# Performance work log

Hardware: AMD Instinct MI355X
Metric: run time of the kernel (lower is better)

The kernel has to match this reference:

```python
import jax, jax.numpy as jnp
import numpy as np

N = 100_000   # nodes
E = 200_000   # directed edges
G = 2_500     # graphs in batch
F_NODE = 16
F_EDGE = 8
H1 = 32
H2 = 16


def setup_inputs() -> dict:
    key = jax.random.key(0)
    ks = jax.random.split(key, 24)
    p = lambda k, shape: 0.1 * jax.random.normal(k, shape, dtype=jnp.float32)
    inp = {
        "x": jax.random.normal(ks[0], (N, F_NODE), dtype=jnp.float32),
        "edge_attr": jax.random.normal(ks[1], (E, F_EDGE), dtype=jnp.float32),
        # edge-MLP for conv1: F_EDGE -> 16 -> F_NODE*H1
        "w_e1a": p(ks[2], (F_EDGE, 16)), "b_e1a": p(ks[3], (16,)),
        "w_e1b": p(ks[4], (16, F_NODE * H1)), "b_e1b": p(ks[5], (F_NODE * H1,)),
        "w_root1": p(ks[6], (F_NODE, H1)), "b_root1": p(ks[7], (H1,)),
        # edge-MLP for conv2: F_EDGE -> 16 -> H1*H2
        "w_e2a": p(ks[8], (F_EDGE, 16)), "b_e2a": p(ks[9], (16,)),
        "w_e2b": p(ks[10], (16, H1 * H2)), "b_e2b": p(ks[11], (H1 * H2,)),
        "w_root2": p(ks[12], (H1, H2)), "b_root2": p(ks[13], (H2,)),
        # attention-pool gate nn: F_NODE -> F_NODE -> 1
        "w_g1": p(ks[14], (F_NODE, F_NODE)), "b_g1": p(ks[15], (F_NODE,)),
        "w_g2": p(ks[16], (F_NODE, 1)), "b_g2": p(ks[17], (1,)),
        # head: (H2 + F_NODE) -> 8 -> 1
        "w_l1": p(ks[18], (H2 + F_NODE, 8)), "b_l1": p(ks[19], (8,)),
        "w_l2": p(ks[20], (8, 1)), "b_l2": p(ks[21], (1,)),
        "edge_index": jax.random.randint(ks[22], (2, E), 0, N),
        "batch": jnp.sort(jax.random.randint(ks[23], (N,), 0, G)),
    }
    return inp


def _nnconv(x, src, tgt, edge_attr, wa, ba, wb, bb, wr, br, in_c, out_c, n):
    # PyG NNConv: x_i' = x_i @ W_root + b + sum_{j->i} x_j @ Theta(e_ji)
    h = jax.nn.relu(edge_attr @ wa + ba)              # [E, 16]
    theta = (h @ wb + bb).reshape(-1, in_c, out_c)    # [E, in, out]
    msg = jnp.einsum('ei,eio->eo', x[src], theta)     # [E, out]
    agg = jax.ops.segment_sum(msg, tgt, num_segments=n)
    return x @ wr + br + agg


def reference(x, edge_attr, w_e1a, b_e1a, w_e1b, b_e1b, w_root1, b_root1,
              w_e2a, b_e2a, w_e2b, b_e2b, w_root2, b_root2,
              w_g1, b_g1, w_g2, b_g2, w_l1, b_l1, w_l2, b_l2,
              edge_index, batch):
    src, tgt = edge_index[0], edge_index[1]
    n = x.shape[0]

    # GlobalAttention pooling on raw node features (per-graph segment softmax)
    gate = jax.nn.relu(x @ w_g1 + b_g1) @ w_g2 + b_g2          # [N, 1]
    m = jax.ops.segment_max(gate, batch, num_segments=G)       # [G, 1]
    a = jnp.exp(gate - m[batch])
    s = jax.ops.segment_sum(a, batch, num_segments=G)
    x_att = jax.ops.segment_sum((a / s[batch]) * x, batch, num_segments=G)  # [G, F_NODE]

    # Two NNConv layers with ReLU
    h = jax.nn.relu(_nnconv(x, src, tgt, edge_attr, w_e1a, b_e1a, w_e1b, b_e1b,
                            w_root1, b_root1, F_NODE, H1, n))
    h = jax.nn.relu(_nnconv(h, src, tgt, edge_attr, w_e2a, b_e2a, w_e2b, b_e2b,
                            w_root2, b_root2, H1, H2, n))

    # global_mean_pool
    cnt = jax.ops.segment_sum(jnp.ones((n, 1), h.dtype), batch, num_segments=G)
    mean = jax.ops.segment_sum(h, batch, num_segments=G) / jnp.maximum(cnt, 1.0)

    z = jnp.concatenate([mean, x_att], axis=1)  # [G, H2 + F_NODE]
    # eval mode: dropout p=0.5 is identity; two linear layers, no activation between
    z = z @ w_l1 + b_l1
    z = z @ w_l2 + b_l2
    return z
```

## Files before the change

### kernel.cpp

```cpp
#include <hip/hip_runtime.h>
#include <hip/hip_bf16.h>

#define NN 100000
#define NE 200000
#define NG 2500
#define FN 16
#define FE 8
#define H1C 32
#define H2C 16
#define KH 16

typedef __attribute__((ext_vector_type(8))) short short8;
typedef __attribute__((ext_vector_type(4))) float f32x4;

__device__ __forceinline__ float bf2f(unsigned int u){
  union { unsigned int i; float f; } v; v.i = (u & 0xffffu) << 16; return v.f;
}
__device__ __forceinline__ unsigned short f2bf(float f){
  union { float f; unsigned int i; } u; u.f = f;
  unsigned int r = u.i + 0x7fffu + ((u.i >> 16) & 1u);
  return (unsigned short)(r >> 16);
}
__device__ __forceinline__ unsigned int pk2(float a, float b){
  return (unsigned int)f2bf(a) | ((unsigned int)f2bf(b) << 16);
}
__device__ __forceinline__ float rdf(const void* p, long i, bool isbf){
  return isbf ? bf2f(((const unsigned short*)p)[i]) : ((const float*)p)[i];
}
__device__ __forceinline__ int lower_bound_i(const int* __restrict__ a, int n, int v){
  int lo = 0, hi = n;
  while(lo < hi){ int mid = (lo + hi) >> 1; if(a[mid] < v) lo = mid + 1; else hi = mid; }
  return lo;
}
__device__ __forceinline__ bool detect_isbf(const void* __restrict__ x){
  const unsigned short* u = (const unsigned short*)x;
  int lane = threadIdx.x & 63;
  float f = bf2f(u[2*lane]);
  float a = fabsf(f);
  bool sane = (f == 0.0f) || (a > 1e-4f && a < 1e4f);
  unsigned long long b = __ballot(sane);
  return __popcll(b) >= 32;
}

#define NW 20
struct WArgs { const void* p[NW]; };
enum {
  OW_E1A=0,     OB_E1A=128,   OW_E1B=144,   OB_E1B=8336,  OW_R1=8848,  OB_R1=9360,
  OW_E2A=9392,  OB_E2A=9520,  OW_E2B=9536,  OB_E2B=17728, OW_R2=18240, OB_R2=18752,
  OW_G1=18768,  OB_G1=19024,  OW_G2=19040,  OB_G2=19056,
  OW_L1=19057,  OB_L1=19313,  OW_L2=19321,  OB_L2=19329
};

#define MB_A 76
#define MB_B (MB_A + 19)
#define MB_C (MB_B + 18)
#define MB_D (MB_C + 391)
#define MB_E (MB_D + 782)
__global__ void __launch_bounds__(256) mega1_kernel(
    const void* __restrict__ xin, const void* __restrict__ efin, WArgs w,
    const int* __restrict__ ei,
    float* __restrict__ wts, unsigned int* __restrict__ wpack1, unsigned int* __restrict__ wpack2,
    float* __restrict__ gate, float* __restrict__ xf, int* __restrict__ deg)
{
  int b = blockIdx.x, tid = threadIdx.x;
  if(b < MB_A){
    bool isbf = detect_isbf(xin);
    int i = b*256 + tid;
    if(i >= 19330) return;
    const int sz[NW] = {128,16,8192,512,512,32, 128,16,8192,512,512,16, 256,16,16,1, 256,8,8,1};
    int seg = 0; long base = 0;
    while(i - base >= sz[seg]){ base += sz[seg]; seg++; }
    wts[i] = rdf(w.p[seg], i - base, isbf);
    return;
  }
  if(b < MB_B){
    bool isbf = detect_isbf(xin);
    int j = (b - MB_A)*256 + tid;
    if(j >= 4736) return;
    int n = j / 148; int k = (j % 148) * 2;
    float v0 = 0.f, v1 = 0.f;
    if(k < 256)        v0 = rdf(w.p[2], (long)k*32 + n, isbf);
    else if(k < 272)   v0 = rdf(w.p[3], (long)(k-256)*32 + n, isbf);
    if(k+1 < 256)      v1 = rdf(w.p[2], (long)(k+1)*32 + n, isbf);
    else if(k+1 < 272) v1 = rdf(w.p[3], (long)(k+1-256)*32 + n, isbf);
    wpack1[j] = pk2(v0, v1);
    return;
  }
  if(b < MB_C){
    bool isbf = detect_isbf(xin);
    int j = (b - MB_B)*256 + tid;
    if(j >= 4416) return;
    int n = j / 276; int k = (j % 276) * 2;
    float v0 = 0.f, v1 = 0.f;
    if(k < 512)        v0 = rdf(w.p[8], (long)k*16 + n, isbf);
    else if(k < 544)   v0 = rdf(w.p[9], (long)(k-512)*16 + n, isbf);
    if(k+1 < 512)      v1 = rdf(w.p[8], (long)(k+1)*16 + n, isbf);
    else if(k+1 < 544) v1 = rdf(w.p[9], (long)(k+1-512)*16 + n, isbf);
    wpack2[j] = pk2(v0, v1);
    return;
  }
  if(b < MB_D){
    __shared__ float s_w1[FN*FN], s_b1[FN], s_w2[FN], s_b2v[1];
    bool isbf = detect_isbf(xin);
    if(tid < FN*FN) s_w1[tid] = rdf(w.p[12], tid, isbf);
    if(tid < FN){ s_b1[tid] = rdf(w.p[13], tid, isbf); s_w2[tid] = rdf(w.p[14], tid, isbf); }
    if(tid == 0) s_b2v[0] = rdf(w.p[15], 0, isbf);
    __syncthreads();
    int n = (b - MB_C)*256 + tid;
    if(n >= NN) return;
    float xv[FN];
    if(isbf){
      uint4 u0 = ((const uint4*)xin)[2*n], u1 = ((const uint4*)xin)[2*n+1];
      xv[0]=bf2f(u0.x); xv[1]=bf2f(u0.x>>16); xv[2]=bf2f(u0.y); xv[3]=bf2f(u0.y>>16);
      xv[4]=bf2f(u0.z); xv[5]=bf2f(u0.z>>16); xv[6]=bf2f(u0.w); xv[7]=bf2f(u0.w>>16);
      xv[8]=bf2f(u1.x); xv[9]=bf2f(u1.x>>16); xv[10]=bf2f(u1.y); xv[11]=bf2f(u1.y>>16);
      xv[12]=bf2f(u1.z); xv[13]=bf2f(u1.z>>16); xv[14]=bf2f(u1.w); xv[15]=bf2f(u1.w>>16);
    } else {
      #pragma unroll
      for(int q = 0; q < 4; q++){
        float4 v = ((const float4*)xin)[4*n + q];
        xv[q*4+0]=v.x; xv[q*4+1]=v.y; xv[q*4+2]=v.z; xv[q*4+3]=v.w;
      }
    }
    float4* xo = (float4*)(xf + (size_t)n*FN);
    #pragma unroll
    for(int q = 0; q < 4; q++) xo[q] = make_float4(xv[q*4+0], xv[q*4+1], xv[q*4+2], xv[q*4+3]);
    float g = s_b2v[0];
    #pragma unroll
    for(int j = 0; j < FN; j++){
      float hj = s_b1[j];
      #pragma unroll
      for(int i = 0; i < FN; i++) hj += xv[i] * s_w1[i*FN + j];
      hj = hj > 0.f ? hj : 0.f;
      g += hj * s_w2[j];
    }
    gate[n] = g;
    return;
  }
  {
    int e = (b - MB_D)*256 + tid;
    if(e < NE) atomicAdd(&deg[ei[NE + e]], 1);
  }
}

#define SCAN_NB 98
__global__ void __launch_bounds__(256) scan_kernel(
    const int* __restrict__ deg, int* __restrict__ rowptr, int* __restrict__ cursor,
    unsigned int* __restrict__ pub)
{
  __shared__ int s_thr[256];
  __shared__ int s_agg[SCAN_NB];
  __shared__ int s_bcast;
  int tid = threadIdx.x, bid = blockIdx.x;
  int base = bid*1024 + tid*4;
  int v0=0, v1=0, v2=0, v3=0;
  if(base + 3 < NN){
    int4 t4 = *(const int4*)(deg + base);
    v0=t4.x; v1=t4.y; v2=t4.z; v3=t4.w;
  } else {
    if(base+0 < NN) v0 = deg[base+0];
    if(base+1 < NN) v1 = deg[base+1];
    if(base+2 < NN) v2 = deg[base+2];
  }
  int e1 = v0, e2 = v0+v1, e3 = v0+v1+v2, tot = v0+v1+v2+v3;
  s_thr[tid] = tot;
  __syncthreads();
  for(int off = 1; off < 256; off <<= 1){
    int t = (tid >= off) ? s_thr[tid-off] : 0;
    __syncthreads();
    s_thr[tid] += t;
    __syncthreads();
  }
  int thr_excl = s_thr[tid] - tot;
  int agg = s_thr[255];
  if(tid == 0) atomicExch(&pub[bid], ((unsigned int)agg << 1) | 1u);
  if(tid < SCAN_NB){
    unsigned int v;
    do { v = atomicAdd(&pub[tid], 0u); } while((v & 1u) == 0u);
    s_agg[tid] = (int)(v >> 1);
  }
  __syncthreads();
  if(tid == 0){
    int acc = 0;
    for(int p = 0; p < bid; p++) acc += s_agg[p];
    s_bcast = acc;
  }
  __syncthreads();
  int ex = s_bcast + thr_excl;
  if(base + 3 < NN){
    int4 r = make_int4(ex, ex+e1, ex+e2, ex+e3);
    *(int4*)(rowptr + base) = r;
    *(int4*)(cursor + base) = r;
  } else {
    if(base+0 < NN){ rowptr[base+0]=ex;    cursor[base+0]=ex;    }
    if(base+1 < NN){ rowptr[base+1]=ex+e1; cursor[base+1]=ex+e1; }
    if(base+2 < NN){ rowptr[base+2]=ex+e2; cursor[base+2]=ex+e2; }
  }
  if(bid == 0 && tid == 0) rowptr[NN] = NE;
}

__global__ void __launch_bounds__(256) fill_edge_kernel(
    const int* __restrict__ ei, int* __restrict__ cursor,
    const void* __restrict__ efin, const float* __restrict__ wts, const void* __restrict__ xin,
    int* __restrict__ srcp, unsigned int* __restrict__ hpk1, unsigned int* __restrict__ hpk2)
{
  __shared__ float s_w1[FE*KH], s_b1[KH], s_w2[FE*KH], s_b2[KH];
  int tid = threadIdx.x;
  if(tid < FE*KH){ s_w1[tid] = wts[OW_E1A + tid]; s_w2[tid] = wts[OW_E2A + tid]; }
  if(tid < KH){ s_b1[tid] = wts[OB_E1A + tid]; s_b2[tid] = wts[OB_E2A + tid]; }
  bool isbf = detect_isbf(xin);
  __syncthreads();
  int e = blockIdx.x*256 + tid;
  if(e >= NE) return;
  int pos = atomicAdd(&cursor[ei[NE + e]], 1);
  srcp[pos] = ei[e];
  float ev[FE];
  if(isbf){
    uint4 u = ((const uint4*)efin)[e];
    ev[0]=bf2f(u.x); ev[1]=bf2f(u.x>>16); ev[2]=bf2f(u.y); ev[3]=bf2f(u.y>>16);
    ev[4]=bf2f(u.z); ev[5]=bf2f(u.z>>16); ev[6]=bf2f(u.w); ev[7]=bf2f(u.w>>16);
  } else {
    float4 a = ((const float4*)efin)[2*e], b = ((const float4*)efin)[2*e+1];
    ev[0]=a.x; ev[1]=a.y; ev[2]=a.z; ev[3]=a.w; ev[4]=b.x; ev[5]=b.y; ev[6]=b.z; ev[7]=b.w;
  }
  unsigned int o[8];
  #pragma unroll
  for(int d = 0; d < 8; d++){
    float h0 = s_b1[2*d], h1 = s_b1[2*d+1];
    #pragma unroll
    for(int k = 0; k < FE; k++){
      h0 += ev[k] * s_w1[k*KH + 2*d];
      h1 += ev[k] * s_w1[k*KH + 2*d+1];
    }
    h0 = h0 > 0.f ? h0 : 0.f; h1 = h1 > 0.f ? h1 : 0.f;
    o[d] = pk2(h0, h1);
  }
  uint4* p1 = (uint4*)(hpk1 + (size_t)pos*8);
  p1[0] = make_uint4(o[0],o[1],o[2],o[3]); p1[1] = make_uint4(o[4],o[5],o[6],o[7]);
  #pragma unroll
  for(int d = 0; d < 8; d++){
    float h0 = s_b2[2*d], h1 = s_b2[2*d+1];
    #pragma unroll
    for(int k = 0; k < FE; k++){
      h0 += ev[k] * s_w2[k*KH + 2*d];
      h1 += ev[k] * s_w2[k*KH + 2*d+1];
    }
    h0 = h0 > 0.f ? h0 : 0.f; h1 = h1 > 0.f ? h1 : 0.f;
    o[d] = pk2(h0, h1);
  }
  uint4* p2 = (uint4*)(hpk2 + (size_t)pos*8);
  p2[0] = make_uint4(o[0],o[1],o[2],o[3]); p2[1] = make_uint4(o[4],o[5],o[6],o[7]);
}

template<int IN, int OUT, bool ABF>
__global__ void __launch_bounds__(256) conv_mfma_kernel(
    const void* __restrict__ nodef, const unsigned int* __restrict__ hpk,
    const int* __restrict__ srcp, const unsigned short* __restrict__ wpack,
    unsigned short* __restrict__ msg)
{
  constexpr int KMF  = ((KH*IN + IN + 31)/32)*32;
  constexpr int KP   = KMF + 8;
  constexpr int NT   = OUT/16;
  constexpr int KS   = KMF/32;
  int tid = threadIdx.x;
  int lane = tid & 63, m = lane & 15, quad = lane >> 4;
  int wid = tid >> 6;
  int ebase = blockIdx.x*64 + wid*16;
  int em = ebase + m;
  int sn = srcp[em];
  int q1 = quad >> 1;
  int xoff = (IN == 16) ? ((quad & 1)*8) : (quad*8);
  float x8[8];
  short8 xb;
  if(ABF){
    uint4 u = *(const uint4*)((const unsigned short*)nodef + (size_t)sn*IN + xoff);
    unsigned int uu[4] = {u.x, u.y, u.z, u.w};
    #pragma unroll
    for(int k = 0; k < 4; k++){ x8[2*k] = bf2f(uu[k]); x8[2*k+1] = bf2f(uu[k] >> 16); }
    xb = *(short8*)&u;
  } else {
    const float4* xp = (const float4*)((const float*)nodef + (size_t)sn*IN + xoff);
    float4 v0 = xp[0], v1 = xp[1];
    x8[0]=v0.x; x8[1]=v0.y; x8[2]=v0.z; x8[3]=v0.w;
    x8[4]=v1.x; x8[5]=v1.y; x8[6]=v1.z; x8[7]=v1.w;
    unsigned int* xbp = (unsigned int*)&xb;
    #pragma unroll
    for(int k = 0; k < 4; k++) xbp[k] = pk2(x8[2*k], x8[2*k+1]);
  }
  unsigned int hu[8];
  {
    const uint4* hp = (const uint4*)(hpk + (size_t)em*8);
    uint4 u0 = hp[0], u1 = hp[1];
    hu[0]=u0.x; hu[1]=u0.y; hu[2]=u0.z; hu[3]=u0.w;
    hu[4]=u1.x; hu[5]=u1.y; hu[6]=u1.z; hu[7]=u1.w;
  }

  f32x4 acc[NT];
  #pragma unroll
  for(int nt = 0; nt < NT; nt++) acc[nt] = (f32x4){0.f,0.f,0.f,0.f};

  #pragma unroll
  for(int ks = 0; ks < KS; ks++){
    short8 a;
    if(ks < KS-1){
      float hv = (IN == 16) ? bf2f(hu[ks] >> (16*q1))
                            : bf2f(hu[ks >> 1] >> (16*(ks & 1)));
      unsigned int* ap = (unsigned int*)&a;
      #pragma unroll
      for(int k = 0; k < 4; k++) ap[k] = pk2(hv*x8[2*k], hv*x8[2*k+1]);
    } else {
      if(IN == 16) a = (quad < 2) ? xb : (short8){0,0,0,0,0,0,0,0};
      else         a = xb;
    }
    #pragma unroll
    for(int nt = 0; nt < NT; nt++){
      short8 b = *(const short8*)(wpack + (size_t)(nt*16 + m)*KP + ks*32 + quad*8);
      acc[nt] = __builtin_amdgcn_mfma_f32_16x16x32_bf16(a, b, acc[nt], 0, 0, 0);
    }
  }
  #pragma unroll
  for(int nt = 0; nt < NT; nt++)
    #pragma unroll
    for(int r = 0; r < 4; r++)
      msg[(size_t)(ebase + quad*4 + r)*OUT + nt*16 + m] = f2bf(acc[nt][r]);
}

__global__ void __launch_bounds__(256) gather1_kernel(
    const float* __restrict__ xf, const unsigned short* __restrict__ msg,
    const int* __restrict__ rowptr,
    const float* __restrict__ wr, const float* __restrict__ br,
    unsigned short* __restrict__ h1b)
{
  __shared__ float s_w[FN*H1C], s_b[H1C];
  for(int i = threadIdx.x; i < FN*H1C; i += 256) s_w[i] = wr[i];
  if(threadIdx.x < H1C) s_b[threadIdx.x] = br[threadIdx.x];
  __syncthreads();
  int g = blockIdx.x*256 + threadIdx.x;
  int n = g >> 3, q = g & 7;
  if(n >= NN) return;
  float a0 = s_b[q*4+0], a1 = s_b[q*4+1], a2 = s_b[q*4+2], a3 = s_b[q*4+3];
  int jb = rowptr[n], je = rowptr[n+1];
  for(int j = jb; j < je; j++){
    const unsigned int* mp = (const unsigned int*)(msg + (size_t)j*H1C + q*4);
    unsigned int u0 = mp[0], u1 = mp[1];
    a0 += bf2f(u0); a1 += bf2f(u0 >> 16); a2 += bf2f(u1); a3 += bf2f(u1 >> 16);
  }
  const float* xr = xf + (size_t)n*FN;
  #pragma unroll
  for(int i = 0; i < FN; i++){
    float xi = xr[i];
    a0 += xi*s_w[i*H1C + q*4+0]; a1 += xi*s_w[i*H1C + q*4+1];
    a2 += xi*s_w[i*H1C + q*4+2]; a3 += xi*s_w[i*H1C + q*4+3];
  }
  a0 = a0>0.f?a0:0.f; a1 = a1>0.f?a1:0.f; a2 = a2>0.f?a2:0.f; a3 = a3>0.f?a3:0.f;
  uint2 hb; hb.x = pk2(a0, a1); hb.y = pk2(a2, a3);
  *(uint2*)(h1b + (size_t)n*H1C + q*4) = hb;
}

__global__ void __launch_bounds__(256) gather2_kernel(
    const unsigned short* __restrict__ h1b, const unsigned short* __restrict__ msg,
    const int* __restrict__ rowptr,
    const float* __restrict__ wr, const float* __restrict__ br, float* __restrict__ h2)
{
  __shared__ float s_w[H1C*H2C], s_b[H2C];
  for(int i = threadIdx.x; i < H1C*H2C; i += 256) s_w[i] = wr[i];
  if(threadIdx.x < H2C) s_b[threadIdx.x] = br[threadIdx.x];
  __syncthreads();
  int g = blockIdx.x*256 + threadIdx.x;
  int n = g >> 2, q = g & 3;
  if(n >= NN) return;
  float a0 = s_b[q*4+0], a1 = s_b[q*4+1], a2 = s_b[q*4+2], a3 = s_b[q*4+3];
  int jb = rowptr[n], je = rowptr[n+1];
  for(int j = jb; j < je; j++){
    const unsigned int* mp = (const unsigned int*)(msg + (size_t)j*H2C + q*4);
    unsigned int u0 = mp[0], u1 = mp[1];
    a0 += bf2f(u0); a1 += bf2f(u0 >> 16); a2 += bf2f(u1); a3 += bf2f(u1 >> 16);
  }
  const unsigned int* hb = (const unsigned int*)(h1b + (size_t)n*H1C);
  #pragma unroll
  for(int i2 = 0; i2 < H1C/2; i2++){
    unsigned int u = hb[i2];
    float x0 = bf2f(u), x1 = bf2f(u >> 16);
    int i = 2*i2;
    a0 += x0*s_w[i*H2C + q*4+0] + x1*s_w[(i+1)*H2C + q*4+0];
    a1 += x0*s_w[i*H2C + q*4+1] + x1*s_w[(i+1)*H2C + q*4+1];
    a2 += x0*s_w[i*H2C + q*4+2] + x1*s_w[(i+1)*H2C + q*4+2];
    a3 += x0*s_w[i*H2C + q*4+3] + x1*s_w[(i+1)*H2C + q*4+3];
  }
  float4 r; r.x = a0>0.f?a0:0.f; r.y = a1>0.f?a1:0.f; r.z = a2>0.f?a2:0.f; r.w = a3>0.f?a3:0.f;
  *(float4*)(h2 + (size_t)n*H2C + q*4) = r;
}

__global__ void head_kernel(const float* __restrict__ gate, const float* __restrict__ xf,
    const float* __restrict__ h2, const int* __restrict__ batch, const void* __restrict__ xin,
    const float* __restrict__ wl1, const float* __restrict__ bl1,
    const float* __restrict__ wl2, const float* __restrict__ bl2,
    void* __restrict__ out)
{
  __shared__ float sz[H2C + FN];
  int g = blockIdx.x;
  int lane = threadIdx.x;
  bool isbf = detect_isbf(xin);
  int start = lower_bound_i(batch, NN, g);
  int end   = lower_bound_i(batch, NN, g + 1);
  float m = -1e30f;
  for(int n = start + lane; n < end; n += 64) m = fmaxf(m, gate[n]);
  #pragma unroll
  for(int o = 32; o >= 1; o >>= 1) m = fmaxf(m, __shfl_xor(m, o));
  float s = 0.f;
  float acc[FN];
  #pragma unroll
  for(int f = 0; f < FN; f++) acc[f] = 0.f;
  for(int n = start + lane; n < end; n += 64){
    float a = __expf(gate[n] - m);
    s += a;
    const float4* xp = (const float4*)(xf + (size_t)n * FN);
    #pragma unroll
    for(int q = 0; q < 4; q++){
      float4 v = xp[q];
      acc[q*4+0] += a*v.x; acc[q*4+1] += a*v.y; acc[q*4+2] += a*v.z; acc[q*4+3] += a*v.w;
    }
  }
  #pragma unroll
  for(int o = 32; o >= 1; o >>= 1){
    s += __shfl_xor(s, o);
    #pragma unroll
    for(int f = 0; f < FN; f++) acc[f] += __shfl_xor(acc[f], o);
  }
  if(lane < FN) sz[H2C + lane] = (end > start && s > 0.f) ? acc[lane] / s : 0.f;
  #pragma unroll
  for(int f = 0; f < H2C; f++) acc[f] = 0.f;
  for(int n = start + lane; n < end; n += 64){
    const float4* hp = (const float4*)(h2 + (size_t)n*H2C);
    #pragma unroll
    for(int q = 0; q < 4; q++){
      float4 v = hp[q];
      acc[q*4+0] += v.x; acc[q*4+1] += v.y; acc[q*4+2] += v.z; acc[q*4+3] += v.w;
    }
  }
  #pragma unroll
  for(int o = 32; o >= 1; o >>= 1){
    #pragma unroll
    for(int f = 0; f < H2C; f++) acc[f] += __shfl_xor(acc[f], o);
  }
  float inv = 1.f / fmaxf((float)(end - start), 1.f);
  if(lane < H2C) sz[lane] = acc[lane] * inv;
  __syncthreads();
  if(lane == 0){
    float t1[8];
    #pragma unroll
    for(int j = 0; j < 8; j++){
      float t = bl1[j];
      #pragma unroll
      for(int c = 0; c < H2C + FN; c++) t += sz[c] * wl1[c*8 + j];
      t1[j] = t;
    }
    float o = bl2[0];
    #pragma unroll
    for(int j = 0; j < 8; j++) o += t1[j] * wl2[j];
    if(isbf) ((__hip_bfloat16*)out)[g] = __float2bfloat16(o);
    else     ((float*)out)[g] = o;
  }
}

extern "C" void kernel_launch(void* const* d_in, const int* in_sizes, int n_in,
                              void* d_out, int out_size, void* d_ws, size_t ws_size,
                              hipStream_t stream)
{
  const int* ei    = (const int*)d_in[22];
  const int* batch = (const int*)d_in[23];

  float* ws = (float*)d_ws;
  float* xf     = ws;
  float* gate   = xf + 1600000;
  float* wts    = gate + 100000;
  int*   rowptr = (int*)(wts + 19360);
  int*   cursor = rowptr + 100016;
  int*   deg    = cursor + 100000;
  unsigned int* pub = (unsigned int*)(deg + 100000);
  int*   srcp   = (int*)(pub + 256);
  unsigned int* wpack1 = (unsigned int*)(srcp + 200000);
  unsigned int* wpack2 = wpack1 + 4736;
  unsigned short* h1b  = (unsigned short*)(wpack2 + 4416);
  unsigned int* hpk1   = (unsigned int*)h1b;
  unsigned short* msg1 = h1b + 3200000;
  unsigned short* msg2 = msg1;
  float* h2     = (float*)(msg1 + 6400000);
  unsigned int* hpk2   = (unsigned int*)h2;

  WArgs wa;
  for(int i = 0; i < NW; i++) wa.p[i] = d_in[2 + i];

  hipMemsetAsync(deg, 0, (100000 + 256)*sizeof(int), stream);
  mega1_kernel<<<MB_E, 256, 0, stream>>>(d_in[0], d_in[1], wa, ei, wts, wpack1, wpack2, gate, xf, deg);
  scan_kernel<<<SCAN_NB, 256, 0, stream>>>(deg, rowptr, cursor, pub);
  fill_edge_kernel<<<(NE + 255)/256, 256, 0, stream>>>(ei, cursor, d_in[1], wts, d_in[0], srcp, hpk1, hpk2);

  conv_mfma_kernel<FN, H1C, false><<<NE/64, 256, 0, stream>>>(
      xf, hpk1, srcp, (const unsigned short*)wpack1, msg1);
  gather1_kernel<<<(NN*8 + 255)/256, 256, 0, stream>>>(xf, msg1, rowptr, wts+OW_R1, wts+OB_R1, h1b);

  conv_mfma_kernel<H1C, H2C, true><<<NE/64, 256, 0, stream>>>(
      h1b, hpk2, srcp, (const unsigned short*)wpack2, msg2);
  gather2_kernel<<<(NN*4 + 255)/256, 256, 0, stream>>>(h1b, msg2, rowptr, wts+OW_R2, wts+OB_R2, h2);

  head_kernel<<<NG, 64, 0, stream>>>(gate, xf, h2, batch, d_in[0],
      wts+OW_L1, wts+OB_L1, wts+OW_L2, wts+OB_L2, d_out);
}
```

Measured before the change: 213.4 us.

## Fuse all stages into one persistent kernel with software grid barriers

Replaces the sequence of seven kernel launches (prep, scan, edge fill, two conv/gather pairs, head) with a single persistent kernel of 512 blocks that grid-strides over each stage and separates stages with an atomic-counter grid barrier. The aim is to remove per-launch overhead and inter-kernel idle gaps between the many short stages. In exchange, each stage now runs on a fixed 512-block grid, which may limit parallelism for stages that had more blocks. The spin barrier assumes all 512 blocks are co-resident (launch bounds allow 2 blocks per CU); if they are not, the kernel deadlocks.

```diff
diff --git a/kernel.cpp b/kernel.cpp
--- a/kernel.cpp
+++ b/kernel.cpp
@@ -9,6 +9,7 @@
 #define H1C 32
 #define H2C 16
 #define KH 16
+#define GB 512
 
 typedef __attribute__((ext_vector_type(8))) short short8;
 typedef __attribute__((ext_vector_type(4))) float f32x4;
@@ -42,6 +43,22 @@
   return __popcll(b) >= 32;
 }
 
+__device__ __forceinline__ void gridbar(int* __restrict__ cnt, int* __restrict__ gen){
+  __syncthreads();
+  if(threadIdx.x == 0){
+    __threadfence();
+    int g = atomicAdd(gen, 0);
+    if(atomicAdd(cnt, 1) == GB-1){
+      atomicExch(cnt, 0);
+      atomicAdd(gen, 1);
+    } else {
+      while(atomicAdd(gen, 0) == g) __builtin_amdgcn_s_sleep(2);
+    }
+    __threadfence();
+  }
+  __syncthreads();
+}
+
 #define NW 20
 struct WArgs { const void* p[NW]; };
 enum {
@@ -50,210 +67,14 @@
   OW_G1=18768,  OB_G1=19024,  OW_G2=19040,  OB_G2=19056,
   OW_L1=19057,  OB_L1=19313,  OW_L2=19321,  OB_L2=19329
 };
-
 #define MB_A 76
 #define MB_B (MB_A + 19)
 #define MB_C (MB_B + 18)
 #define MB_D (MB_C + 391)
-#define MB_E (MB_D + 782)
-__global__ void __launch_bounds__(256) mega1_kernel(
-    const void* __restrict__ xin, const void* __restrict__ efin, WArgs w,
-    const int* __restrict__ ei,
-    float* __restrict__ wts, unsigned int* __restrict__ wpack1, unsigned int* __restrict__ wpack2,
-    float* __restrict__ gate, float* __restrict__ xf, int* __restrict__ deg)
-{
-  int b = blockIdx.x, tid = threadIdx.x;
-  if(b < MB_A){
-    bool isbf = detect_isbf(xin);
-    int i = b*256 + tid;
-    if(i >= 19330) return;
-    const int sz[NW] = {128,16,8192,512,512,32, 128,16,8192,512,512,16, 256,16,16,1, 256,8,8,1};
-    int seg = 0; long base = 0;
-    while(i - base >= sz[seg]){ base += sz[seg]; seg++; }
-    wts[i] = rdf(w.p[seg], i - base, isbf);
-    return;
-  }
-  if(b < MB_B){
-    bool isbf = detect_isbf(xin);
-    int j = (b - MB_A)*256 + tid;
-    if(j >= 4736) return;
-    int n = j / 148; int k = (j % 148) * 2;
-    float v0 = 0.f, v1 = 0.f;
-    if(k < 256)        v0 = rdf(w.p[2], (long)k*32 + n, isbf);
-    else if(k < 272)   v0 = rdf(w.p[3], (long)(k-256)*32 + n, isbf);
-    if(k+1 < 256)      v1 = rdf(w.p[2], (long)(k+1)*32 + n, isbf);
-    else if(k+1 < 272) v1 = rdf(w.p[3], (long)(k+1-256)*32 + n, isbf);
-    wpack1[j] = pk2(v0, v1);
-    return;
-  }
-  if(b < MB_C){
-    bool isbf = detect_isbf(xin);
-    int j = (b - MB_B)*256 + tid;
-    if(j >= 4416) return;
-    int n = j / 276; int k = (j % 276) * 2;
-    float v0 = 0.f, v1 = 0.f;
-    if(k < 512)        v0 = rdf(w.p[8], (long)k*16 + n, isbf);
-    else if(k < 544)   v0 = rdf(w.p[9], (long)(k-512)*16 + n, isbf);
-    if(k+1 < 512)      v1 = rdf(w.p[8], (long)(k+1)*16 + n, isbf);
-    else if(k+1 < 544) v1 = rdf(w.p[9], (long)(k+1-512)*16 + n, isbf);
-    wpack2[j] = pk2(v0, v1);
-    return;
-  }
-  if(b < MB_D){
-    __shared__ float s_w1[FN*FN], s_b1[FN], s_w2[FN], s_b2v[1];
-    bool isbf = detect_isbf(xin);
-    if(tid < FN*FN) s_w1[tid] = rdf(w.p[12], tid, isbf);
-    if(tid < FN){ s_b1[tid] = rdf(w.p[13], tid, isbf); s_w2[tid] = rdf(w.p[14], tid, isbf); }
-    if(tid == 0) s_b2v[0] = rdf(w.p[15], 0, isbf);
-    __syncthreads();
-    int n = (b - MB_C)*256 + tid;
-    if(n >= NN) return;
-    float xv[FN];
-    if(isbf){
-      uint4 u0 = ((const uint4*)xin)[2*n], u1 = ((const uint4*)xin)[2*n+1];
-      xv[0]=bf2f(u0.x); xv[1]=bf2f(u0.x>>16); xv[2]=bf2f(u0.y); xv[3]=bf2f(u0.y>>16);
-      xv[4]=bf2f(u0.z); xv[5]=bf2f(u0.z>>16); xv[6]=bf2f(u0.w); xv[7]=bf2f(u0.w>>16);
-      xv[8]=bf2f(u1.x); xv[9]=bf2f(u1.x>>16); xv[10]=bf2f(u1.y); xv[11]=bf2f(u1.y>>16);
-      xv[12]=bf2f(u1.z); xv[13]=bf2f(u1.z>>16); xv[14]=bf2f(u1.w); xv[15]=bf2f(u1.w>>16);
-    } else {
-      #pragma unroll
-      for(int q = 0; q < 4; q++){
-        float4 v = ((const float4*)xin)[4*n + q];
-        xv[q*4+0]=v.x; xv[q*4+1]=v.y; xv[q*4+2]=v.z; xv[q*4+3]=v.w;
-      }
-    }
-    float4* xo = (float4*)(xf + (size_t)n*FN);
-    #pragma unroll
-    for(int q = 0; q < 4; q++) xo[q] = make_float4(xv[q*4+0], xv[q*4+1], xv[q*4+2], xv[q*4+3]);
-    float g = s_b2v[0];
-    #pragma unroll
-    for(int j = 0; j < FN; j++){
-      float hj = s_b1[j];
-      #pragma unroll
-      for(int i = 0; i < FN; i++) hj += xv[i] * s_w1[i*FN + j];
-      hj = hj > 0.f ? hj : 0.f;
-      g += hj * s_w2[j];
-    }
-    gate[n] = g;
-    return;
-  }
-  {
-    int e = (b - MB_D)*256 + tid;
-    if(e < NE) atomicAdd(&deg[ei[NE + e]], 1);
-  }
-}
-
-#define SCAN_NB 98
-__global__ void __launch_bounds__(256) scan_kernel(
-    const int* __restrict__ deg, int* __restrict__ rowptr, int* __restrict__ cursor,
-    unsigned int* __restrict__ pub)
-{
-  __shared__ int s_thr[256];
-  __shared__ int s_agg[SCAN_NB];
-  __shared__ int s_bcast;
-  int tid = threadIdx.x, bid = blockIdx.x;
-  int base = bid*1024 + tid*4;
-  int v0=0, v1=0, v2=0, v3=0;
-  if(base + 3 < NN){
-    int4 t4 = *(const int4*)(deg + base);
-    v0=t4.x; v1=t4.y; v2=t4.z; v3=t4.w;
-  } else {
-    if(base+0 < NN) v0 = deg[base+0];
-    if(base+1 < NN) v1 = deg[base+1];
-    if(base+2 < NN) v2 = deg[base+2];
-  }
-  int e1 = v0, e2 = v0+v1, e3 = v0+v1+v2, tot = v0+v1+v2+v3;
-  s_thr[tid] = tot;
-  __syncthreads();
-  for(int off = 1; off < 256; off <<= 1){
-    int t = (tid >= off) ? s_thr[tid-off] : 0;
-    __syncthreads();
-    s_thr[tid] += t;
-    __syncthreads();
-  }
-  int thr_excl = s_thr[tid] - tot;
-  int agg = s_thr[255];
-  if(tid == 0) atomicExch(&pub[bid], ((unsigned int)agg << 1) | 1u);
-  if(tid < SCAN_NB){
-    unsigned int v;
-    do { v = atomicAdd(&pub[tid], 0u); } while((v & 1u) == 0u);
-    s_agg[tid] = (int)(v >> 1);
-  }
-  __syncthreads();
-  if(tid == 0){
-    int acc = 0;
-    for(int p = 0; p < bid; p++) acc += s_agg[p];
-    s_bcast = acc;
-  }
-  __syncthreads();
-  int ex = s_bcast + thr_excl;
-  if(base + 3 < NN){
-    int4 r = make_int4(ex, ex+e1, ex+e2, ex+e3);
-    *(int4*)(rowptr + base) = r;
-    *(int4*)(cursor + base) = r;
-  } else {
-    if(base+0 < NN){ rowptr[base+0]=ex;    cursor[base+0]=ex;    }
-    if(base+1 < NN){ rowptr[base+1]=ex+e1; cursor[base+1]=ex+e1; }
-    if(base+2 < NN){ rowptr[base+2]=ex+e2; cursor[base+2]=ex+e2; }
-  }
-  if(bid == 0 && tid == 0) rowptr[NN] = NE;
-}
-
-__global__ void __launch_bounds__(256) fill_edge_kernel(
-    const int* __restrict__ ei, int* __restrict__ cursor,
-    const void* __restrict__ efin, const float* __restrict__ wts, const void* __restrict__ xin,
-    int* __restrict__ srcp, unsigned int* __restrict__ hpk1, unsigned int* __restrict__ hpk2)
-{
-  __shared__ float s_w1[FE*KH], s_b1[KH], s_w2[FE*KH], s_b2[KH];
-  int tid = threadIdx.x;
-  if(tid < FE*KH){ s_w1[tid] = wts[OW_E1A + tid]; s_w2[tid] = wts[OW_E2A + tid]; }
-  if(tid < KH){ s_b1[tid] = wts[OB_E1A + tid]; s_b2[tid] = wts[OB_E2A + tid]; }
-  bool isbf = detect_isbf(xin);
-  __syncthreads();
-  int e = blockIdx.x*256 + tid;
-  if(e >= NE) return;
-  int pos = atomicAdd(&cursor[ei[NE + e]], 1);
-  srcp[pos] = ei[e];
-  float ev[FE];
-  if(isbf){
-    uint4 u = ((const uint4*)efin)[e];
-    ev[0]=bf2f(u.x); ev[1]=bf2f(u.x>>16); ev[2]=bf2f(u.y); ev[3]=bf2f(u.y>>16);
-    ev[4]=bf2f(u.z); ev[5]=bf2f(u.z>>16); ev[6]=bf2f(u.w); ev[7]=bf2f(u.w>>16);
-  } else {
-    float4 a = ((const float4*)efin)[2*e], b = ((const float4*)efin)[2*e+1];
-    ev[0]=a.x; ev[1]=a.y; ev[2]=a.z; ev[3]=a.w; ev[4]=b.x; ev[5]=b.y; ev[6]=b.z; ev[7]=b.w;
-  }
-  unsigned int o[8];
-  #pragma unroll
-  for(int d = 0; d < 8; d++){
-    float h0 = s_b1[2*d], h1 = s_b1[2*d+1];
-    #pragma unroll
-    for(int k = 0; k < FE; k++){
-      h0 += ev[k] * s_w1[k*KH + 2*d];
-      h1 += ev[k] * s_w1[k*KH + 2*d+1];
-    }
-    h0 = h0 > 0.f ? h0 : 0.f; h1 = h1 > 0.f ? h1 : 0.f;
-    o[d] = pk2(h0, h1);
-  }
-  uint4* p1 = (uint4*)(hpk1 + (size_t)pos*8);
-  p1[0] = make_uint4(o[0],o[1],o[2],o[3]); p1[1] = make_uint4(o[4],o[5],o[6],o[7]);
-  #pragma unroll
-  for(int d = 0; d < 8; d++){
-    float h0 = s_b2[2*d], h1 = s_b2[2*d+1];
-    #pragma unroll
-    for(int k = 0; k < FE; k++){
-      h0 += ev[k] * s_w2[k*KH + 2*d];
-      h1 += ev[k] * s_w2[k*KH + 2*d+1];
-    }
-    h0 = h0 > 0.f ? h0 : 0.f; h1 = h1 > 0.f ? h1 : 0.f;
-    o[d] = pk2(h0, h1);
-  }
-  uint4* p2 = (uint4*)(hpk2 + (size_t)pos*8);
-  p2[0] = make_uint4(o[0],o[1],o[2],o[3]); p2[1] = make_uint4(o[4],o[5],o[6],o[7]);
-}
+#define CHUNK 196
 
 template<int IN, int OUT, bool ABF>
-__global__ void __launch_bounds__(256) conv_mfma_kernel(
+__device__ __forceinline__ void conv_unit(int u, int tid,
     const void* __restrict__ nodef, const unsigned int* __restrict__ hpk,
     const int* __restrict__ srcp, const unsigned short* __restrict__ wpack,
     unsigned short* __restrict__ msg)
@@ -262,10 +83,9 @@
   constexpr int KP   = KMF + 8;
   constexpr int NT   = OUT/16;
   constexpr int KS   = KMF/32;
-  int tid = threadIdx.x;
   int lane = tid & 63, m = lane & 15, quad = lane >> 4;
   int wid = tid >> 6;
-  int ebase = blockIdx.x*64 + wid*16;
+  int ebase = u*64 + wid*16;
   int em = ebase + m;
   int sn = srcp[em];
   int q1 = quad >> 1;
@@ -273,11 +93,11 @@
   float x8[8];
   short8 xb;
   if(ABF){
-    uint4 u = *(const uint4*)((const unsigned short*)nodef + (size_t)sn*IN + xoff);
-    unsigned int uu[4] = {u.x, u.y, u.z, u.w};
+    uint4 uu4 = *(const uint4*)((const unsigned short*)nodef + (size_t)sn*IN + xoff);
+    unsigned int uu[4] = {uu4.x, uu4.y, uu4.z, uu4.w};
     #pragma unroll
     for(int k = 0; k < 4; k++){ x8[2*k] = bf2f(uu[k]); x8[2*k+1] = bf2f(uu[k] >> 16); }
-    xb = *(short8*)&u;
+    xb = *(short8*)&uu4;
   } else {
     const float4* xp = (const float4*)((const float*)nodef + (size_t)sn*IN + xoff);
     float4 v0 = xp[0], v1 = xp[1];
@@ -294,11 +114,9 @@
     hu[0]=u0.x; hu[1]=u0.y; hu[2]=u0.z; hu[3]=u0.w;
     hu[4]=u1.x; hu[5]=u1.y; hu[6]=u1.z; hu[7]=u1.w;
   }
-
   f32x4 acc[NT];
   #pragma unroll
   for(int nt = 0; nt < NT; nt++) acc[nt] = (f32x4){0.f,0.f,0.f,0.f};
-
   #pragma unroll
   for(int ks = 0; ks < KS; ks++){
     short8 a;
@@ -314,8 +132,8 @@
     }
     #pragma unroll
     for(int nt = 0; nt < NT; nt++){
-      short8 b = *(const short8*)(wpack + (size_t)(nt*16 + m)*KP + ks*32 + quad*8);
-      acc[nt] = __builtin_amdgcn_mfma_f32_16x16x32_bf16(a, b, acc[nt], 0, 0, 0);
+      short8 bfr = *(const short8*)(wpack + (size_t)(nt*16 + m)*KP + ks*32 + quad*8);
+      acc[nt] = __builtin_amdgcn_mfma_f32_16x16x32_bf16(a, bfr, acc[nt], 0, 0, 0);
     }
   }
   #pragma unroll
@@ -325,141 +143,322 @@
       msg[(size_t)(ebase + quad*4 + r)*OUT + nt*16 + m] = f2bf(acc[nt][r]);
 }
 
-__global__ void __launch_bounds__(256) gather1_kernel(
-    const float* __restrict__ xf, const unsigned short* __restrict__ msg,
-    const int* __restrict__ rowptr,
-    const float* __restrict__ wr, const float* __restrict__ br,
-    unsigned short* __restrict__ h1b)
+__global__ void __launch_bounds__(256, 2) mega_kernel(
+    const void* __restrict__ xin, const void* __restrict__ efin, WArgs w,
+    const int* __restrict__ ei, const int* __restrict__ batch,
+    float* __restrict__ wts, unsigned int* __restrict__ wpack1, unsigned int* __restrict__ wpack2,
+    float* __restrict__ gate, float* __restrict__ xf,
+    int* __restrict__ deg, int* __restrict__ partials, int* __restrict__ bar,
+    int* __restrict__ rowptr, int* __restrict__ cursor, int* __restrict__ srcp,
+    unsigned int* __restrict__ hpk1, unsigned int* __restrict__ hpk2,
+    unsigned short* __restrict__ h1b, unsigned short* __restrict__ msg,
+    float* __restrict__ h2, void* __restrict__ out)
 {
-  __shared__ float s_w[FN*H1C], s_b[H1C];
-  for(int i = threadIdx.x; i < FN*H1C; i += 256) s_w[i] = wr[i];
-  if(threadIdx.x < H1C) s_b[threadIdx.x] = br[threadIdx.x];
-  __syncthreads();
-  int g = blockIdx.x*256 + threadIdx.x;
-  int n = g >> 3, q = g & 7;
-  if(n >= NN) return;
-  float a0 = s_b[q*4+0], a1 = s_b[q*4+1], a2 = s_b[q*4+2], a3 = s_b[q*4+3];
-  int jb = rowptr[n], je = rowptr[n+1];
-  for(int j = jb; j < je; j++){
-    const unsigned int* mp = (const unsigned int*)(msg + (size_t)j*H1C + q*4);
-    unsigned int u0 = mp[0], u1 = mp[1];
-    a0 += bf2f(u0); a1 += bf2f(u0 >> 16); a2 += bf2f(u1); a3 += bf2f(u1 >> 16);
-  }
-  const float* xr = xf + (size_t)n*FN;
-  #pragma unroll
-  for(int i = 0; i < FN; i++){
-    float xi = xr[i];
-    a0 += xi*s_w[i*H1C + q*4+0]; a1 += xi*s_w[i*H1C + q*4+1];
-    a2 += xi*s_w[i*H1C + q*4+2]; a3 += xi*s_w[i*H1C + q*4+3];
-  }
-  a0 = a0>0.f?a0:0.f; a1 = a1>0.f?a1:0.f; a2 = a2>0.f?a2:0.f; a3 = a3>0.f?a3:0.f;
-  uint2 hb; hb.x = pk2(a0, a1); hb.y = pk2(a2, a3);
-  *(uint2*)(h1b + (size_t)n*H1C + q*4) = hb;
-}
-
-__global__ void __launch_bounds__(256) gather2_kernel(
-    const unsigned short* __restrict__ h1b, const unsigned short* __restrict__ msg,
-    const int* __restrict__ rowptr,
-    const float* __restrict__ wr, const float* __restrict__ br, float* __restrict__ h2)
-{
-  __shared__ float s_w[H1C*H2C], s_b[H2C];
-  for(int i = threadIdx.x; i < H1C*H2C; i += 256) s_w[i] = wr[i];
-  if(threadIdx.x < H2C) s_b[threadIdx.x] = br[threadIdx.x];
-  __syncthreads();
-  int g = blockIdx.x*256 + threadIdx.x;
-  int n = g >> 2, q = g & 3;
-  if(n >= NN) return;
-  float a0 = s_b[q*4+0], a1 = s_b[q*4+1], a2 = s_b[q*4+2], a3 = s_b[q*4+3];
-  int jb = rowptr[n], je = rowptr[n+1];
-  for(int j = jb; j < je; j++){
-    const unsigned int* mp = (const unsigned int*)(msg + (size_t)j*H2C + q*4);
-    unsigned int u0 = mp[0], u1 = mp[1];
-    a0 += bf2f(u0); a1 += bf2f(u0 >> 16); a2 += bf2f(u1); a3 += bf2f(u1 >> 16);
-  }
-  const unsigned int* hb = (const unsigned int*)(h1b + (size_t)n*H1C);
-  #pragma unroll
-  for(int i2 = 0; i2 < H1C/2; i2++){
-    unsigned int u = hb[i2];
-    float x0 = bf2f(u), x1 = bf2f(u >> 16);
-    int i = 2*i2;
-    a0 += x0*s_w[i*H2C + q*4+0] + x1*s_w[(i+1)*H2C + q*4+0];
-    a1 += x0*s_w[i*H2C + q*4+1] + x1*s_w[(i+1)*H2C + q*4+1];
-    a2 += x0*s_w[i*H2C + q*4+2] + x1*s_w[(i+1)*H2C + q*4+2];
-    a3 += x0*s_w[i*H2C + q*4+3] + x1*s_w[(i+1)*H2C + q*4+3];
-  }
-  float4 r; r.x = a0>0.f?a0:0.f; r.y = a1>0.f?a1:0.f; r.z = a2>0.f?a2:0.f; r.w = a3>0.f?a3:0.f;
-  *(float4*)(h2 + (size_t)n*H2C + q*4) = r;
-}
-
-__global__ void head_kernel(const float* __restrict__ gate, const float* __restrict__ xf,
-    const float* __restrict__ h2, const int* __restrict__ batch, const void* __restrict__ xin,
-    const float* __restrict__ wl1, const float* __restrict__ bl1,
-    const float* __restrict__ wl2, const float* __restrict__ bl2,
-    void* __restrict__ out)
-{
-  __shared__ float sz[H2C + FN];
-  int g = blockIdx.x;
-  int lane = threadIdx.x;
+  __shared__ int   s_i[512];
+  __shared__ float s_f[512];
+  __shared__ float s_f2[64];
+  __shared__ float s_hd[4*48];
+  int b = blockIdx.x, tid = threadIdx.x;
+  int* cnt = bar; int* gen = bar + 4;
   bool isbf = detect_isbf(xin);
-  int start = lower_bound_i(batch, NN, g);
-  int end   = lower_bound_i(batch, NN, g + 1);
-  float m = -1e30f;
-  for(int n = start + lane; n < end; n += 64) m = fmaxf(m, gate[n]);
-  #pragma unroll
-  for(int o = 32; o >= 1; o >>= 1) m = fmaxf(m, __shfl_xor(m, o));
-  float s = 0.f;
-  float acc[FN];
-  #pragma unroll
-  for(int f = 0; f < FN; f++) acc[f] = 0.f;
-  for(int n = start + lane; n < end; n += 64){
-    float a = __expf(gate[n] - m);
-    s += a;
-    const float4* xp = (const float4*)(xf + (size_t)n * FN);
-    #pragma unroll
-    for(int q = 0; q < 4; q++){
-      float4 v = xp[q];
-      acc[q*4+0] += a*v.x; acc[q*4+1] += a*v.y; acc[q*4+2] += a*v.z; acc[q*4+3] += a*v.w;
-    }
-  }
-  #pragma unroll
-  for(int o = 32; o >= 1; o >>= 1){
-    s += __shfl_xor(s, o);
-    #pragma unroll
-    for(int f = 0; f < FN; f++) acc[f] += __shfl_xor(acc[f], o);
-  }
-  if(lane < FN) sz[H2C + lane] = (end > start && s > 0.f) ? acc[lane] / s : 0.f;
-  #pragma unroll
-  for(int f = 0; f < H2C; f++) acc[f] = 0.f;
-  for(int n = start + lane; n < end; n += 64){
-    const float4* hp = (const float4*)(h2 + (size_t)n*H2C);
-    #pragma unroll
-    for(int q = 0; q < 4; q++){
-      float4 v = hp[q];
-      acc[q*4+0] += v.x; acc[q*4+1] += v.y; acc[q*4+2] += v.z; acc[q*4+3] += v.w;
-    }
-  }
-  #pragma unroll
-  for(int o = 32; o >= 1; o >>= 1){
-    #pragma unroll
-    for(int f = 0; f < H2C; f++) acc[f] += __shfl_xor(acc[f], o);
-  }
-  float inv = 1.f / fmaxf((float)(end - start), 1.f);
-  if(lane < H2C) sz[lane] = acc[lane] * inv;
-  __syncthreads();
-  if(lane == 0){
-    float t1[8];
-    #pragma unroll
-    for(int j = 0; j < 8; j++){
-      float t = bl1[j];
-      #pragma unroll
-      for(int c = 0; c < H2C + FN; c++) t += sz[c] * wl1[c*8 + j];
-      t1[j] = t;
-    }
-    float o = bl2[0];
-    #pragma unroll
-    for(int j = 0; j < 8; j++) o += t1[j] * wl2[j];
-    if(isbf) ((__hip_bfloat16*)out)[g] = __float2bfloat16(o);
-    else     ((float*)out)[g] = o;
+
+  if(b < MB_A){
+    int i = b*256 + tid;
+    if(i < 19330){
+      const int sz[NW] = {128,16,8192,512,512,32, 128,16,8192,512,512,16, 256,16,16,1, 256,8,8,1};
+      int seg = 0; long base = 0;
+      while(i - base >= sz[seg]){ base += sz[seg]; seg++; }
+      wts[i] = rdf(w.p[seg], i - base, isbf);
+    }
+  } else if(b < MB_B){
+    int j = (b - MB_A)*256 + tid;
+    if(j < 4736){
+      int n = j / 148; int k = (j % 148) * 2;
+      float v0 = 0.f, v1 = 0.f;
+      if(k < 256)        v0 = rdf(w.p[2], (long)k*32 + n, isbf);
+      else if(k < 272)   v0 = rdf(w.p[3], (long)(k-256)*32 + n, isbf);
+      if(k+1 < 256)      v1 = rdf(w.p[2], (long)(k+1)*32 + n, isbf);
+      else if(k+1 < 272) v1 = rdf(w.p[3], (long)(k+1-256)*32 + n, isbf);
+      wpack1[j] = pk2(v0, v1);
+    }
+  } else if(b < MB_C){
+    int j = (b - MB_B)*256 + tid;
+    if(j < 4416){
+      int n = j / 276; int k = (j % 276) * 2;
+      float v0 = 0.f, v1 = 0.f;
+      if(k < 512)        v0 = rdf(w.p[8], (long)k*16 + n, isbf);
+      else if(k < 544)   v0 = rdf(w.p[9], (long)(k-512)*16 + n, isbf);
+      if(k+1 < 512)      v1 = rdf(w.p[8], (long)(k+1)*16 + n, isbf);
+      else if(k+1 < 544) v1 = rdf(w.p[9], (long)(k+1-512)*16 + n, isbf);
+      wpack2[j] = pk2(v0, v1);
+    }
+  } else if(b < MB_D){
+    if(tid < FN*FN) s_f[tid] = rdf(w.p[12], tid, isbf);
+    if(tid < FN){ s_f2[tid] = rdf(w.p[13], tid, isbf); s_f2[32 + tid] = rdf(w.p[14], tid, isbf); }
+    if(tid == 0) s_f2[63] = rdf(w.p[15], 0, isbf);
+    __syncthreads();
+    int n = (b - MB_C)*256 + tid;
+    if(n < NN){
+      float xv[FN];
+      if(isbf){
+        uint4 u0 = ((const uint4*)xin)[2*n], u1 = ((const uint4*)xin)[2*n+1];
+        xv[0]=bf2f(u0.x); xv[1]=bf2f(u0.x>>16); xv[2]=bf2f(u0.y); xv[3]=bf2f(u0.y>>16);
+        xv[4]=bf2f(u0.z); xv[5]=bf2f(u0.z>>16); xv[6]=bf2f(u0.w); xv[7]=bf2f(u0.w>>16);
+        xv[8]=bf2f(u1.x); xv[9]=bf2f(u1.x>>16); xv[10]=bf2f(u1.y); xv[11]=bf2f(u1.y>>16);
+        xv[12]=bf2f(u1.z); xv[13]=bf2f(u1.z>>16); xv[14]=bf2f(u1.w); xv[15]=bf2f(u1.w>>16);
+      } else {
+        #pragma unroll
+        for(int q = 0; q < 4; q++){
+          float4 v = ((const float4*)xin)[4*n + q];
+          xv[q*4+0]=v.x; xv[q*4+1]=v.y; xv[q*4+2]=v.z; xv[q*4+3]=v.w;
+        }
+      }
+      float4* xo = (float4*)(xf + (size_t)n*FN);
+      #pragma unroll
+      for(int q = 0; q < 4; q++) xo[q] = make_float4(xv[q*4+0], xv[q*4+1], xv[q*4+2], xv[q*4+3]);
+      float g = s_f2[63];
+      #pragma unroll
+      for(int j = 0; j < FN; j++){
+        float hj = s_f2[j];
+        #pragma unroll
+        for(int i = 0; i < FN; i++) hj += xv[i] * s_f[i*FN + j];
+        hj = hj > 0.f ? hj : 0.f;
+        g += hj * s_f2[32 + j];
+      }
+      gate[n] = g;
+    }
+  }
+  for(int t = b*256 + tid; t < NE; t += GB*256) atomicAdd(&deg[ei[NE + t]], 1);
+  gridbar(cnt, gen);
+
+  {
+    int base = b*CHUNK;
+    int v = (tid < CHUNK && base + tid < NN) ? deg[base + tid] : 0;
+    s_i[tid] = v;
+    __syncthreads();
+    for(int off = 128; off > 0; off >>= 1){
+      if(tid < off) s_i[tid] += s_i[tid + off];
+      __syncthreads();
+    }
+    if(tid == 0) partials[b] = s_i[0];
+  }
+  gridbar(cnt, gen);
+  if(b == 0){
+    s_i[tid] = partials[tid]; s_i[tid + 256] = partials[tid + 256];
+    __syncthreads();
+    for(int off = 1; off < 512; off <<= 1){
+      int v0 = (tid >= off) ? s_i[tid - off] : 0;
+      int v1 = (tid + 256 >= off) ? s_i[tid + 256 - off] : 0;
+      __syncthreads();
+      s_i[tid] += v0; s_i[tid + 256] += v1;
+      __syncthreads();
+    }
+    partials[tid]       = (tid == 0) ? 0 : s_i[tid - 1];
+    partials[tid + 256] = s_i[tid + 255];
+  }
+  gridbar(cnt, gen);
+  {
+    int base = b*CHUNK;
+    int v = (tid < CHUNK && base + tid < NN) ? deg[base + tid] : 0;
+    s_i[tid] = v;
+    __syncthreads();
+    for(int off = 1; off < 256; off <<= 1){
+      int t = (tid >= off) ? s_i[tid - off] : 0;
+      __syncthreads();
+      s_i[tid] += t;
+      __syncthreads();
+    }
+    int excl = partials[b] + s_i[tid] - v;
+    if(tid < CHUNK && base + tid < NN){ rowptr[base + tid] = excl; cursor[base + tid] = excl; }
+    if(b == 0 && tid == 0) rowptr[NN] = NE;
+  }
+  gridbar(cnt, gen);
+
+  {
+    __syncthreads();
+    if(tid < FE*KH){ s_f[tid] = wts[OW_E1A + tid]; s_f[128 + tid] = wts[OW_E2A + tid]; }
+    if(tid < KH){ s_f2[tid] = wts[OB_E1A + tid]; s_f2[16 + tid] = wts[OB_E2A + tid]; }
+    __syncthreads();
+    for(int e = b*256 + tid; e < NE; e += GB*256){
+      int pos = atomicAdd(&cursor[ei[NE + e]], 1);
+      srcp[pos] = ei[e];
+      float ev[FE];
+      if(isbf){
+        uint4 u = ((const uint4*)efin)[e];
+        ev[0]=bf2f(u.x); ev[1]=bf2f(u.x>>16); ev[2]=bf2f(u.y); ev[3]=bf2f(u.y>>16);
+        ev[4]=bf2f(u.z); ev[5]=bf2f(u.z>>16); ev[6]=bf2f(u.w); ev[7]=bf2f(u.w>>16);
+      } else {
+        float4 a = ((const float4*)efin)[2*e], bb = ((const float4*)efin)[2*e+1];
+        ev[0]=a.x; ev[1]=a.y; ev[2]=a.z; ev[3]=a.w; ev[4]=bb.x; ev[5]=bb.y; ev[6]=bb.z; ev[7]=bb.w;
+      }
+      unsigned int o[8];
+      #pragma unroll
+      for(int d = 0; d < 8; d++){
+        float h0 = s_f2[2*d], h1 = s_f2[2*d+1];
+        #pragma unroll
+        for(int k = 0; k < FE; k++){
+          h0 += ev[k] * s_f[k*KH + 2*d];
+          h1 += ev[k] * s_f[k*KH + 2*d+1];
+        }
+        h0 = h0 > 0.f ? h0 : 0.f; h1 = h1 > 0.f ? h1 : 0.f;
+        o[d] = pk2(h0, h1);
+      }
+      uint4* p1 = (uint4*)(hpk1 + (size_t)pos*8);
+      p1[0] = make_uint4(o[0],o[1],o[2],o[3]); p1[1] = make_uint4(o[4],o[5],o[6],o[7]);
+      #pragma unroll
+      for(int d = 0; d < 8; d++){
+        float h0 = s_f2[16 + 2*d], h1 = s_f2[16 + 2*d+1];
+        #pragma unroll
+        for(int k = 0; k < FE; k++){
+          h0 += ev[k] * s_f[128 + k*KH + 2*d];
+          h1 += ev[k] * s_f[128 + k*KH + 2*d+1];
+        }
+        h0 = h0 > 0.f ? h0 : 0.f; h1 = h1 > 0.f ? h1 : 0.f;
+        o[d] = pk2(h0, h1);
+      }
+      uint4* p2 = (uint4*)(hpk2 + (size_t)pos*8);
+      p2[0] = make_uint4(o[0],o[1],o[2],o[3]); p2[1] = make_uint4(o[4],o[5],o[6],o[7]);
+    }
+  }
+  gridbar(cnt, gen);
+
+  for(int u = b; u < NE/64; u += GB)
+    conv_unit<FN, H1C, false>(u, tid, xf, hpk1, srcp, (const unsigned short*)wpack1, msg);
+  gridbar(cnt, gen);
+
+  {
+    __syncthreads();
+    for(int i = tid; i < FN*H1C; i += 256) s_f[i] = wts[OW_R1 + i];
+    if(tid < H1C) s_f2[tid] = wts[OB_R1 + tid];
+    __syncthreads();
+    for(int u = b; u < NN*8/256; u += GB){
+      int g = u*256 + tid;
+      int n = g >> 3, q = g & 7;
+      if(n < NN){
+        float a0 = s_f2[q*4+0], a1 = s_f2[q*4+1], a2 = s_f2[q*4+2], a3 = s_f2[q*4+3];
+        int jb = rowptr[n], je = rowptr[n+1];
+        for(int j = jb; j < je; j++){
+          const unsigned int* mp = (const unsigned int*)(msg + (size_t)j*H1C + q*4);
+          unsigned int u0 = mp[0], u1 = mp[1];
+          a0 += bf2f(u0); a1 += bf2f(u0 >> 16); a2 += bf2f(u1); a3 += bf2f(u1 >> 16);
+        }
+        const float* xr = xf + (size_t)n*FN;
+        #pragma unroll
+        for(int i = 0; i < FN; i++){
+          float xi = xr[i];
+          a0 += xi*s_f[i*H1C + q*4+0]; a1 += xi*s_f[i*H1C + q*4+1];
+          a2 += xi*s_f[i*H1C + q*4+2]; a3 += xi*s_f[i*H1C + q*4+3];
+        }
+        a0 = a0>0.f?a0:0.f; a1 = a1>0.f?a1:0.f; a2 = a2>0.f?a2:0.f; a3 = a3>0.f?a3:0.f;
+        uint2 hb; hb.x = pk2(a0, a1); hb.y = pk2(a2, a3);
+        *(uint2*)(h1b + (size_t)n*H1C + q*4) = hb;
+      }
+    }
+  }
+  gridbar(cnt, gen);
+
+  for(int u = b; u < NE/64; u += GB)
+    conv_unit<H1C, H2C, true>(u, tid, h1b, hpk2, srcp, (const unsigned short*)wpack2, msg);
+  gridbar(cnt, gen);
+
+  {
+    __syncthreads();
+    for(int i = tid; i < H1C*H2C; i += 256) s_f[i] = wts[OW_R2 + i];
+    if(tid < H2C) s_f2[tid] = wts[OB_R2 + tid];
+    __syncthreads();
+    for(int u = b; u < (NN*4 + 255)/256; u += GB){
+      int g = u*256 + tid;
+      int n = g >> 2, q = g & 3;
+      if(n < NN){
+        float a0 = s_f2[q*4+0], a1 = s_f2[q*4+1], a2 = s_f2[q*4+2], a3 = s_f2[q*4+3];
+        int jb = rowptr[n], je = rowptr[n+1];
+        for(int j = jb; j < je; j++){
+          const unsigned int* mp = (const unsigned int*)(msg + (size_t)j*H2C + q*4);
+          unsigned int u0 = mp[0], u1 = mp[1];
+          a0 += bf2f(u0); a1 += bf2f(u0 >> 16); a2 += bf2f(u1); a3 += bf2f(u1 >> 16);
+        }
+        const unsigned int* hb = (const unsigned int*)(h1b + (size_t)n*H1C);
+        #pragma unroll
+        for(int i2 = 0; i2 < H1C/2; i2++){
+          unsigned int u2 = hb[i2];
+          float x0 = bf2f(u2), x1 = bf2f(u2 >> 16);
+          int i = 2*i2;
+          a0 += x0*s_f[i*H2C + q*4+0] + x1*s_f[(i+1)*H2C + q*4+0];
+          a1 += x0*s_f[i*H2C + q*4+1] + x1*s_f[(i+1)*H2C + q*4+1];
+          a2 += x0*s_f[i*H2C + q*4+2] + x1*s_f[(i+1)*H2C + q*4+2];
+          a3 += x0*s_f[i*H2C + q*4+3] + x1*s_f[(i+1)*H2C + q*4+3];
+        }
+        float4 r; r.x = a0>0.f?a0:0.f; r.y = a1>0.f?a1:0.f; r.z = a2>0.f?a2:0.f; r.w = a3>0.f?a3:0.f;
+        *(float4*)(h2 + (size_t)n*H2C + q*4) = r;
+      }
+    }
+  }
+  gridbar(cnt, gen);
+
+  {
+    int wid = tid >> 6, lane = tid & 63;
+    float* sz = s_hd + wid*48;
+    for(int g = b*4 + wid; g < NG; g += GB*4){
+      int start = lower_bound_i(batch, NN, g);
+      int end   = lower_bound_i(batch, NN, g + 1);
+      float m = -1e30f;
+      for(int n = start + lane; n < end; n += 64) m = fmaxf(m, gate[n]);
+      #pragma unroll
+      for(int o = 32; o >= 1; o >>= 1) m = fmaxf(m, __shfl_xor(m, o));
+      float s = 0.f;
+      float acc[FN];
+      #pragma unroll
+      for(int f = 0; f < FN; f++) acc[f] = 0.f;
+      for(int n = start + lane; n < end; n += 64){
+        float a = __expf(gate[n] - m);
+        s += a;
+        const float4* xp = (const float4*)(xf + (size_t)n * FN);
+        #pragma unroll
+        for(int q = 0; q < 4; q++){
+          float4 v = xp[q];
+          acc[q*4+0] += a*v.x; acc[q*4+1] += a*v.y; acc[q*4+2] += a*v.z; acc[q*4+3] += a*v.w;
+        }
+      }
+      #pragma unroll
+      for(int o = 32; o >= 1; o >>= 1){
+        s += __shfl_xor(s, o);
+        #pragma unroll
+        for(int f = 0; f < FN; f++) acc[f] += __shfl_xor(acc[f], o);
+      }
+      if(lane < FN) sz[H2C + lane] = (end > start && s > 0.f) ? acc[lane] / s : 0.f;
+      #pragma unroll
+      for(int f = 0; f < H2C; f++) acc[f] = 0.f;
+      for(int n = start + lane; n < end; n += 64){
+        const float4* hp = (const float4*)(h2 + (size_t)n*H2C);
+        #pragma unroll
+        for(int q = 0; q < 4; q++){
+          float4 v = hp[q];
+          acc[q*4+0] += v.x; acc[q*4+1] += v.y; acc[q*4+2] += v.z; acc[q*4+3] += v.w;
+        }
+      }
+      #pragma unroll
+      for(int o = 32; o >= 1; o >>= 1){
+        #pragma unroll
+        for(int f = 0; f < H2C; f++) acc[f] += __shfl_xor(acc[f], o);
+      }
+      float inv = 1.f / fmaxf((float)(end - start), 1.f);
+      if(lane < H2C) sz[lane] = acc[lane] * inv;
+      if(lane == 0){
+        float t1[8];
+        #pragma unroll
+        for(int j = 0; j < 8; j++){
+          float t = wts[OB_L1 + j];
+          #pragma unroll
+          for(int c = 0; c < H2C + FN; c++) t += sz[c] * wts[OW_L1 + c*8 + j];
+          t1[j] = t;
+        }
+        float o = wts[OB_L2];
+        #pragma unroll
+        for(int j = 0; j < 8; j++) o += t1[j] * wts[OW_L2 + j];
+        if(isbf) ((__hip_bfloat16*)out)[g] = __float2bfloat16(o);
+        else     ((float*)out)[g] = o;
+      }
+    }
   }
 }
 
@@ -477,33 +476,24 @@
   int*   rowptr = (int*)(wts + 19360);
   int*   cursor = rowptr + 100016;
   int*   deg    = cursor + 100000;
-  unsigned int* pub = (unsigned int*)(deg + 100000);
-  int*   srcp   = (int*)(pub + 256);
+  int*   partials = deg + 100000;
+  int*   bar    = partials + 512;
+  int*   srcp   = bar + 16;
   unsigned int* wpack1 = (unsigned int*)(srcp + 200000);
   unsigned int* wpack2 = wpack1 + 4736;
   unsigned short* h1b  = (unsigned short*)(wpack2 + 4416);
   unsigned int* hpk1   = (unsigned int*)h1b;
-  unsigned short* msg1 = h1b + 3200000;
-  unsigned short* msg2 = msg1;
-  float* h2     = (float*)(msg1 + 6400000);
+  unsigned short* msg  = h1b + 3200000;
+  float* h2     = (float*)(msg + 6400000);
   unsigned int* hpk2   = (unsigned int*)h2;
 
   WArgs wa;
   for(int i = 0; i < NW; i++) wa.p[i] = d_in[2 + i];
 
-  hipMemsetAsync(deg, 0, (100000 + 256)*sizeof(int), stream);
-  mega1_kernel<<<MB_E, 256, 0, stream>>>(d_in[0], d_in[1], wa, ei, wts, wpack1, wpack2, gate, xf, deg);
-  scan_kernel<<<SCAN_NB, 256, 0, stream>>>(deg, rowptr, cursor, pub);
-  fill_edge_kernel<<<(NE + 255)/256, 256, 0, stream>>>(ei, cursor, d_in[1], wts, d_in[0], srcp, hpk1, hpk2);
-
-  conv_mfma_kernel<FN, H1C, false><<<NE/64, 256, 0, stream>>>(
-      xf, hpk1, srcp, (const unsigned short*)wpack1, msg1);
-  gather1_kernel<<<(NN*8 + 255)/256, 256, 0, stream>>>(xf, msg1, rowptr, wts+OW_R1, wts+OB_R1, h1b);
-
-  conv_mfma_kernel<H1C, H2C, true><<<NE/64, 256, 0, stream>>>(
-      h1b, hpk2, srcp, (const unsigned short*)wpack2, msg2);
-  gather2_kernel<<<(NN*4 + 255)/256, 256, 0, stream>>>(h1b, msg2, rowptr, wts+OW_R2, wts+OB_R2, h2);
-
-  head_kernel<<<NG, 64, 0, stream>>>(gate, xf, h2, batch, d_in[0],
-      wts+OW_L1, wts+OB_L1, wts+OW_L2, wts+OB_L2, d_out);
-}
+  hipMemsetAsync(deg, 0, (100000 + 512 + 16)*sizeof(int), stream);
+  mega_kernel<<<GB, 256, 0, stream>>>(
+      d_in[0], d_in[1], wa, ei, batch,
+      wts, wpack1, wpack2, gate, xf,
+      deg, partials, bar, rowptr, cursor, srcp,
+      hpk1, hpk2, h1b, msg, h2, d_out);
+}
```

New measurement: 701.9 us. +229.0%, slower.
